# Optimization experiments

Measured on AMD Instinct MI355X. Metric: run time of the kernel, lower is better.

Reference implementation:

```python
import jax, jax.numpy as jnp
import numpy as np

N, E, IN, OUT = 50000, 1600000, 64, 64
DIM, K = 2, 5          # pseudo-coordinate dim, kernel size per dim
KP = K ** DIM          # 25 kernel weight matrices
S = 2 ** DIM           # 4 non-zero linear B-spline basis products per edge
# bit pattern per basis product: bits[s, d] in {0,1}
_BITS = np.array([[(s >> d) & 1 for d in range(DIM)] for s in range(S)], dtype=np.int32)
_OFFS = np.array([K ** (DIM - 1 - d) for d in range(DIM)], dtype=np.int32)  # row-major flatten


def setup_inputs() -> dict:
    key = jax.random.key(0)
    ks = jax.random.split(key, 6)
    x = jax.random.normal(ks[0], (N, IN), dtype=jnp.float32)
    edge_index = jax.random.randint(ks[1], (2, E), 0, N)
    pseudo = jax.random.uniform(ks[2], (E, DIM), dtype=jnp.float32)
    bnd = 1.0 / np.sqrt(KP * IN)  # matches uniform(size) init in reset_parameters
    weight = jax.random.uniform(ks[3], (KP, IN, OUT), dtype=jnp.float32, minval=-bnd, maxval=bnd)
    root_weight = jax.random.uniform(ks[4], (IN, OUT), dtype=jnp.float32, minval=-bnd, maxval=bnd)
    bias = jax.random.uniform(ks[5], (OUT,), dtype=jnp.float32, minval=-bnd, maxval=bnd)
    return {"x": x, "edge_index": edge_index, "pseudo": pseudo,
            "weight": weight, "root_weight": root_weight, "bias": bias}


def _basis_and_index(pseudo):
    # open B-spline, degree 1: scale by (K - 1)
    v = pseudo * jnp.asarray(K - 1, pseudo.dtype)          # [E, DIM]
    lo = jnp.floor(v)
    frac = v - lo                                          # [E, DIM]
    lo = lo.astype(jnp.int32)
    bits = jnp.asarray(_BITS)                              # [S, DIM]
    # basis[e, s] = prod_d (frac if bit else 1-frac)
    terms = jnp.where(bits[None].astype(bool), frac[:, None, :], 1.0 - frac[:, None, :])
    basis = jnp.prod(terms, axis=-1)                       # [E, S]
    idx_d = (lo[:, None, :] + bits[None]) % K              # [E, S, DIM]; wrap is harmless (basis=0 there)
    idx = jnp.sum(idx_d * jnp.asarray(_OFFS), axis=-1)     # [E, S] flat weight index in [0, KP)
    return basis, idx


def reference(x, edge_index, pseudo, weight, root_weight, bias):
    row, col = edge_index[0], edge_index[1]                # row = target, col = source
    basis, idx = _basis_and_index(pseudo)                  # [E,S], [E,S]
    x_src = x[col]                                         # [E, IN] gather
    # Accumulate basis-weighted source features per (target node, kernel index),
    # then apply the dense [KP, IN, OUT] weights once (same math, no [E,IN,OUT] blowup).
    acc = jnp.zeros((N * KP, IN), x.dtype)
    for s in range(S):  # S=4, fixed structural loop
        acc = acc + jax.ops.segment_sum(basis[:, s:s + 1] * x_src,
                                        row * KP + idx[:, s], num_segments=N * KP)
    out = jnp.einsum('nki,kio->no', acc.reshape(N, KP, IN), weight)  # [N, OUT]
    deg = jax.ops.segment_sum(jnp.ones((E,), x.dtype), row, num_segments=N)
    out = out / jnp.clip(deg, 1.0)[:, None]                # mean over neighbors (1/N(i))
    return out + x @ root_weight + bias
```

## Files before the change

### kernel.cpp

```cpp
#include <hip/hip_runtime.h>
#include <hip/hip_fp16.h>
#include <hip/hip_bf16.h>


#define NN    50000
#define EE    1600000
#define NPB   16
#define KD    1664
#define ASTB  1672
#define OFCAP 16384

#define NB    391
#define NSH   4
#define CCAP  1280
#define CSTR  16

#define REC_B 6250
#define XB_B  1563
#define WT_B  104

typedef unsigned short ushort_t;
typedef unsigned long long u64_t;
typedef __attribute__((ext_vector_type(8))) short short8;
typedef __attribute__((ext_vector_type(4))) float f32x4;

static __device__ __forceinline__ ushort_t f2bf(float f) {
  union { float f; unsigned u; } v; v.f = f;
  return (ushort_t)((v.u + 0x7fffu + ((v.u >> 16) & 1u)) >> 16);
}
static __device__ __forceinline__ unsigned pk2bf(float a, float b) {
  __hip_bfloat162 h = __float22bfloat162_rn(make_float2(a, b));
  union { __hip_bfloat162 h; unsigned u; } cv; cv.h = h; return cv.u;
}
union S8 { short8 s; unsigned u[4]; };

__global__ __launch_bounds__(256) void k_prep(
    const int* __restrict__ ei, const float* __restrict__ pseudo,
    int* __restrict__ ccur, uint2* __restrict__ coarse,
    const float* __restrict__ x, ushort_t* __restrict__ xb,
    const float* __restrict__ w, const float* __restrict__ root,
    ushort_t* __restrict__ wt, int useXB) {
  const int b = blockIdx.x;
  const int tid = threadIdx.x;
  if (b < REC_B) {
    int e = b * 256 + tid;
    int row = ei[e], col = ei[EE + e];
    float2 pv = ((const float2*)pseudo)[e];
    float v0 = pv.x * 4.0f, v1 = pv.y * 4.0f;
    unsigned h0 = __half_as_ushort(__float2half(v0));
    unsigned h1 = __half_as_ushort(__float2half(v1));
    int c4 = (row >> 7) * NSH + (tid & (NSH - 1));
    int slot = atomicAdd(&ccur[c4 * CSTR], 1);
    if (slot < CCAP)
      coarse[(size_t)c4 * CCAP + slot] =
          make_uint2((unsigned)col | ((unsigned)(row & 127) << 16), h0 | (h1 << 16));
  } else if (b < REC_B + XB_B) {
    if (!useXB) return;
    int t = (b - REC_B) * 256 + tid;
    if (t < NN * 8) {
      const float4* xp = (const float4*)x + (size_t)t * 2;
      float4 aa = xp[0], bb = xp[1];
      S8 o;
      o.u[0] = pk2bf(aa.x, aa.y); o.u[1] = pk2bf(aa.z, aa.w);
      o.u[2] = pk2bf(bb.x, bb.y); o.u[3] = pk2bf(bb.z, bb.w);
      ((short8*)xb)[t] = o.s;
    }
  } else {
    int t = (b - REC_B - XB_B) * 256 + tid;
    int idx = t * 4;
    if (idx < 64 * KD) {
      int o = idx / KD, k = idx - o * KD;
#pragma unroll
      for (int q = 0; q < 4; ++q) {
        int kk = k + q;
        int kp = kk >> 6, c = kk & 63;
        int fi = 4 * (c & 15) + (c >> 4);
        wt[idx + q] = (kp < 25) ? f2bf(w[(kp * 64 + fi) * 64 + o])
                                : f2bf(root[fi * 64 + o]);
      }
    }
  }
}

__global__ __launch_bounds__(256) void k_sort(
    const int* __restrict__ ccur, const uint2* __restrict__ coarse,
    uint2* __restrict__ recs2, int* __restrict__ degA,
    uint4* __restrict__ ofl, int* __restrict__ ofc) {
  __shared__ int cnt[128], lpos[128];
  const int c = blockIdx.x, tid = threadIdx.x;
  if (tid < 128) cnt[tid] = 0;
  __syncthreads();
  const int pc = c * NSH;
  for (int s = 0; s < NSH; ++s) {
    int n = min(ccur[(pc + s) * CSTR], CCAP);
    const uint2* seg = coarse + (size_t)(pc + s) * CCAP;
    for (int i = tid; i < n; i += 256) atomicAdd(&cnt[(seg[i].x >> 16) & 127], 1);
  }
  __syncthreads();
  if (tid < 128) {
    int row = c * 128 + tid;
    lpos[tid] = row * 64;
    if (row < NN) degA[row] = cnt[tid];
  }
  for (int i = tid; i < 128 * 64; i += 256) {
    int r7 = i >> 6, sl = i & 63;
    int row = c * 128 + r7;
    if (row < NN && sl >= cnt[r7])
      recs2[(size_t)row * 64 + sl] = make_uint2(0u, 0x7C007C00u);
  }
  __syncthreads();
  for (int s = 0; s < NSH; ++s) {
    int n = min(ccur[(pc + s) * CSTR], CCAP);
    const uint2* seg = coarse + (size_t)(pc + s) * CCAP;
    for (int i = tid; i < n; i += 256) {
      uint2 r = seg[i];
      int r7 = (r.x >> 16) & 127;
      int dst = atomicAdd(&lpos[r7], 1);
      int sl = dst - (c * 128 + r7) * 64;
      if (sl < 64) {
        recs2[dst] = make_uint2(r.x & 0xFFFFu, r.y);
      } else {
        int o = atomicAdd(ofc, 1);
        if (o < OFCAP) {
          float v0 = __half2float(__ushort_as_half((ushort_t)(r.y & 0xFFFFu)));
          float v1 = __half2float(__ushort_as_half((ushort_t)(r.y >> 16)));
          ofl[o] = make_uint4((unsigned)(c * 128 + r7), r.x & 0xFFFFu,
                              __float_as_uint(v0), __float_as_uint(v1));
        }
      }
    }
  }
}

static __device__ __forceinline__ void issue8(
    const ushort_t* __restrict__ xb, const unsigned (&vo)[8], u64_t (&g)[8]) {
  asm volatile(
      "global_load_dwordx2 %[o0], %[a0], %[sb]\n\t"
      "global_load_dwordx2 %[o1], %[a1], %[sb]\n\t"
      "global_load_dwordx2 %[o2], %[a2], %[sb]\n\t"
      "global_load_dwordx2 %[o3], %[a3], %[sb]\n\t"
      "global_load_dwordx2 %[o4], %[a4], %[sb]\n\t"
      "global_load_dwordx2 %[o5], %[a5], %[sb]\n\t"
      "global_load_dwordx2 %[o6], %[a6], %[sb]\n\t"
      "global_load_dwordx2 %[o7], %[a7], %[sb]\n\t"
      : [o0] "=&v"(g[0]), [o1] "=&v"(g[1]), [o2] "=&v"(g[2]), [o3] "=&v"(g[3]),
        [o4] "=&v"(g[4]), [o5] "=&v"(g[5]), [o6] "=&v"(g[6]), [o7] "=&v"(g[7])
      : [a0] "v"(vo[0]), [a1] "v"(vo[1]), [a2] "v"(vo[2]), [a3] "v"(vo[3]),
        [a4] "v"(vo[4]), [a5] "v"(vo[5]), [a6] "v"(vo[6]), [a7] "v"(vo[7]),
        [sb] "s"(xb));
}
static __device__ __forceinline__ void wait8(u64_t (&g)[8]) {
  asm volatile("s_waitcnt vmcnt(0)"
               : "+v"(g[0]), "+v"(g[1]), "+v"(g[2]), "+v"(g[3]),
                 "+v"(g[4]), "+v"(g[5]), "+v"(g[6]), "+v"(g[7]));
}

static __device__ __forceinline__ void vo8(
    unsigned wx, int base, int quad, int m15, unsigned (&vo)[8]) {
#pragma unroll
  for (int j = 0; j < 8; ++j) {
    unsigned c = (unsigned)__shfl((int)wx, base + quad * 8 + j);
    vo[j] = (c << 7) + (unsigned)(m15 << 3);
  }
}

static __device__ __forceinline__ void hats8(
    unsigned wy, int base, int quad, int m15,
    float r0f, float c0f, float r1f, float c1f, S8& aT0, S8& aT1) {
#pragma unroll
  for (int p = 0; p < 4; ++p) {
    float a0[2], a1[2];
#pragma unroll
    for (int q = 0; q < 2; ++q) {
      unsigned pv = (unsigned)__shfl((int)wy, base + quad * 8 + 2 * p + q);
      float v0 = __half2float(__ushort_as_half((ushort_t)(pv & 0xFFFFu)));
      float v1 = __half2float(__ushort_as_half((ushort_t)(pv >> 16)));
      a0[q] = fmaxf(0.f, 1.f - fabsf(v0 - r0f)) * fmaxf(0.f, 1.f - fabsf(v1 - c0f));
      a1[q] = fmaxf(0.f, 1.f - fabsf(v0 - r1f)) * fmaxf(0.f, 1.f - fabsf(v1 - c1f));
    }
    aT0.u[p] = pk2bf(a0[0], a0[1]);
    aT1.u[p] = pk2bf(a1[0], a1[1]);
  }
}

static __device__ __forceinline__ void packmfma(
    const u64_t (&g)[8], const S8& aT0, const S8& aT1, f32x4 (&acc)[2][4]) {
  S8 bT[4];
#pragma unroll
  for (int p = 0; p < 4; ++p) {
    unsigned lo0 = (unsigned)g[2 * p],     hi0 = (unsigned)(g[2 * p] >> 32);
    unsigned lo1 = (unsigned)g[2 * p + 1], hi1 = (unsigned)(g[2 * p + 1] >> 32);
    bT[0].u[p] = (lo0 & 0xFFFFu) | (lo1 << 16);
    bT[1].u[p] = (lo0 >> 16)     | (lo1 & 0xFFFF0000u);
    bT[2].u[p] = (hi0 & 0xFFFFu) | (hi1 << 16);
    bT[3].u[p] = (hi0 >> 16)     | (hi1 & 0xFFFF0000u);
  }
  __builtin_amdgcn_s_setprio(1);
#pragma unroll
  for (int t = 0; t < 4; ++t) {
    acc[0][t] = __builtin_amdgcn_mfma_f32_16x16x32_bf16(aT0.s, bT[t].s, acc[0][t], 0, 0, 0);
    acc[1][t] = __builtin_amdgcn_mfma_f32_16x16x32_bf16(aT1.s, bT[t].s, acc[1][t], 0, 0, 0);
  }
  __builtin_amdgcn_s_setprio(0);
}

static __device__ __forceinline__ void node_bf16(
    unsigned wx, unsigned wy, int m, int quad, int m15,
    float r0f, float c0f, float r1f, float c1f,
    const ushort_t* __restrict__ xb, f32x4 (&acc)[2][4]) {
  if (m > 32) {
    unsigned vo0[8], vo1[8];
    u64_t g0[8], g1[8];
    vo8(wx, 0, quad, m15, vo0);
    issue8(xb, vo0, g0);
    vo8(wx, 32, quad, m15, vo1);
    issue8(xb, vo1, g1);
    S8 aT0_0, aT1_0, aT0_1, aT1_1;
    hats8(wy, 0,  quad, m15, r0f, c0f, r1f, c1f, aT0_0, aT1_0);
    hats8(wy, 32, quad, m15, r0f, c0f, r1f, c1f, aT0_1, aT1_1);
    __builtin_amdgcn_sched_barrier(0);
    wait8(g0); wait8(g1);
    packmfma(g0, aT0_0, aT1_0, acc);
    packmfma(g1, aT0_1, aT1_1, acc);
  } else {
    unsigned vo0[8];
    u64_t g0[8];
    vo8(wx, 0, quad, m15, vo0);
    issue8(xb, vo0, g0);
    S8 aT0, aT1;
    hats8(wy, 0, quad, m15, r0f, c0f, r1f, c1f, aT0, aT1);
    __builtin_amdgcn_sched_barrier(0);
    wait8(g0);
    packmfma(g0, aT0, aT1, acc);
  }
}

static __device__ __forceinline__ void replay_ofl(
    const uint4* __restrict__ ofl, int ofcv, int node, int quad, int m15,
    float r0f, float c0f, float r1f, float c1f,
    const float* __restrict__ x, f32x4 (&acc)[2][4]) {
  for (int i = 0; i < ofcv; ++i) {
    uint4 r = ofl[i];
    if ((int)r.x != node) continue;
    float v0 = __uint_as_float(r.z), v1 = __uint_as_float(r.w);
    float h00 = fmaxf(0.f, 1.f - fabsf(v0 - r0f));
    float h01 = fmaxf(0.f, 1.f - fabsf(v1 - c0f));
    float h10 = fmaxf(0.f, 1.f - fabsf(v0 - r1f));
    float h11 = fmaxf(0.f, 1.f - fabsf(v1 - c1f));
    float mk = (quad == 0) ? 1.0f : 0.0f;
    S8 aT0, aT1, bT[4];
#pragma unroll
    for (int p = 0; p < 4; ++p) { aT0.u[p] = 0; aT1.u[p] = 0; }
    aT0.u[0] = pk2bf(h00 * h01 * mk, 0.0f);
    aT1.u[0] = pk2bf(h10 * h11 * mk, 0.0f);
    float4 xv = *(const float4*)(x + (size_t)r.y * 64 + (m15 << 2));
    float fv[4] = {xv.x, xv.y, xv.z, xv.w};
#pragma unroll
    for (int t = 0; t < 4; ++t)
#pragma unroll
      for (int p = 0; p < 4; ++p) bT[t].u[p] = pk2bf(fv[t], fv[t]);
#pragma unroll
    for (int t = 0; t < 4; ++t) {
      acc[0][t] = __builtin_amdgcn_mfma_f32_16x16x32_bf16(aT0.s, bT[t].s, acc[0][t], 0, 0, 0);
      acc[1][t] = __builtin_amdgcn_mfma_f32_16x16x32_bf16(aT1.s, bT[t].s, acc[1][t], 0, 0, 0);
    }
  }
}

static __device__ __forceinline__ void do_chunk_f32(
    const uint2 (&rq)[8], int kb, int m, int quad, int m15,
    float r0f, float c0f, float r1f, float c1f,
    const float* __restrict__ x, f32x4 (&acc)[2][4]) {
  unsigned cj[8], pj[8];
#pragma unroll
  for (int j = 0; j < 8; ++j) {
    cj[j] = min(rq[j].x, (unsigned)(NN - 1));
    pj[j] = rq[j].y;
  }
  float gf[4][8];
#pragma unroll
  for (int j = 0; j < 8; ++j) {
    float4 v = *(const float4*)(x + ((size_t)cj[j] << 6) + (m15 << 2));
    gf[0][j] = v.x; gf[1][j] = v.y; gf[2][j] = v.z; gf[3][j] = v.w;
  }
  S8 aT0, aT1, bT[4];
#pragma unroll
  for (int p = 0; p < 4; ++p) {
    float a0[2], a1[2];
#pragma unroll
    for (int q = 0; q < 2; ++q) {
      int j = 2 * p + q;
      unsigned pv = pj[j];
      float v0 = __half2float(__ushort_as_half((ushort_t)(pv & 0xFFFFu)));
      float v1 = __half2float(__ushort_as_half((ushort_t)(pv >> 16)));
      bool ok = (kb + quad * 8 + j) < m;
      float p0 = fmaxf(0.f, 1.f - fabsf(v0 - r0f)) * fmaxf(0.f, 1.f - fabsf(v1 - c0f));
      float p1 = fmaxf(0.f, 1.f - fabsf(v0 - r1f)) * fmaxf(0.f, 1.f - fabsf(v1 - c1f));
      a0[q] = ok ? p0 : 0.0f;
      a1[q] = ok ? p1 : 0.0f;
    }
    aT0.u[p] = pk2bf(a0[0], a0[1]);
    aT1.u[p] = pk2bf(a1[0], a1[1]);
  }
#pragma unroll
  for (int p = 0; p < 4; ++p)
#pragma unroll
    for (int t = 0; t < 4; ++t)
      bT[t].u[p] = pk2bf(gf[t][2 * p], gf[t][2 * p + 1]);
#pragma unroll
  for (int t = 0; t < 4; ++t) {
    acc[0][t] = __builtin_amdgcn_mfma_f32_16x16x32_bf16(aT0.s, bT[t].s, acc[0][t], 0, 0, 0);
    acc[1][t] = __builtin_amdgcn_mfma_f32_16x16x32_bf16(aT1.s, bT[t].s, acc[1][t], 0, 0, 0);
  }
}

static __device__ __forceinline__ void spill_acc(
    ushort_t* accS, int row, int quad, int m15, const f32x4 (&acc)[2][4]) {
#pragma unroll
  for (int mt = 0; mt < 2; ++mt)
#pragma unroll
    for (int r = 0; r < 4; ++r) {
      int kp = mt * 16 + quad * 4 + r;
      if (kp < 25) {
#pragma unroll
        for (int nt = 0; nt < 4; ++nt)
          accS[row * ASTB + kp * 64 + nt * 16 + m15] = f2bf(acc[mt][nt][r]);
      }
    }
}

template <bool XBF>
__global__ __launch_bounds__(512, 4) void k_main(
    const uint2* __restrict__ recs2, const int* __restrict__ degA,
    const uint4* __restrict__ ofl, const int* __restrict__ ofc,
    const float* __restrict__ x, const ushort_t* __restrict__ xb,
    const ushort_t* __restrict__ wt, const float* __restrict__ bias,
    float* __restrict__ out) {
  __shared__ ushort_t accS[NPB * ASTB];
  __shared__ float    outp[2 * NPB * 64];
  __shared__ float    sinv[NPB];
  const int tid = threadIdx.x;
  const int lane = tid & 63;
  const int w = tid >> 6;
  const int nb = blockIdx.x * NPB;

  const int m15 = lane & 15, quad = lane >> 4;
  const float r0f = (float)(m15 / 5),        c0f = (float)(m15 % 5);
  const float r1f = (float)((16 + m15) / 5), c1f = (float)((16 + m15) % 5);
  const int fl = 4 * m15 + quad;

  const int rowA = w << 1, rowB = rowA + 1;
  const int nodeA = nb + rowA, nodeB = nb + rowB;

  const int mA = degA[nodeA], mB = degA[nodeB];
  uint2 wA = recs2[(size_t)nodeA * 64 + lane];
  uint2 wB = recs2[(size_t)nodeB * 64 + lane];
  const float rxA = x[(size_t)nodeA * 64 + fl];
  const float rxB = x[(size_t)nodeB * 64 + fl];
  const int ofcv = min(ofc[0], OFCAP);

  const float dcfA = (float)max(mA, 1), dcfB = (float)max(mB, 1);
  if (lane == 0) { sinv[rowA] = 1.0f / dcfA; sinv[rowB] = 1.0f / dcfB; }
  accS[rowA * ASTB + 1600 + lane] = f2bf(rxA * dcfA);
  accS[rowB * ASTB + 1600 + lane] = f2bf(rxB * dcfB);

  f32x4 acc[2][4];
#pragma unroll
  for (int a = 0; a < 2; ++a)
#pragma unroll
    for (int b = 0; b < 4; ++b) acc[a][b] = (f32x4){0.f, 0.f, 0.f, 0.f};

  if (XBF) {
    node_bf16(wA.x, wA.y, mA, quad, m15, r0f, c0f, r1f, c1f, xb, acc);
    if (ofcv) replay_ofl(ofl, ofcv, nodeA, quad, m15, r0f, c0f, r1f, c1f, x, acc);
    spill_acc(accS, rowA, quad, m15, acc);
#pragma unroll
    for (int a = 0; a < 2; ++a)
#pragma unroll
      for (int b = 0; b < 4; ++b) acc[a][b] = (f32x4){0.f, 0.f, 0.f, 0.f};
    node_bf16(wB.x, wB.y, mB, quad, m15, r0f, c0f, r1f, c1f, xb, acc);
    if (ofcv) replay_ofl(ofl, ofcv, nodeB, quad, m15, r0f, c0f, r1f, c1f, x, acc);
    spill_acc(accS, rowB, quad, m15, acc);
  } else {
    for (int e0 = 0; e0 < min(mA, 64); e0 += 32) {
      uint2 rq[8];
#pragma unroll
      for (int j = 0; j < 8; ++j) rq[j] = recs2[(size_t)nodeA * 64 + e0 + quad * 8 + j];
      do_chunk_f32(rq, e0, mA, quad, m15, r0f, c0f, r1f, c1f, x, acc);
    }
    if (ofcv) replay_ofl(ofl, ofcv, nodeA, quad, m15, r0f, c0f, r1f, c1f, x, acc);
    spill_acc(accS, rowA, quad, m15, acc);
#pragma unroll
    for (int a = 0; a < 2; ++a)
#pragma unroll
      for (int b = 0; b < 4; ++b) acc[a][b] = (f32x4){0.f, 0.f, 0.f, 0.f};
    for (int e0 = 0; e0 < min(mB, 64); e0 += 32) {
      uint2 rq[8];
#pragma unroll
      for (int j = 0; j < 8; ++j) rq[j] = recs2[(size_t)nodeB * 64 + e0 + quad * 8 + j];
      do_chunk_f32(rq, e0, mB, quad, m15, r0f, c0f, r1f, c1f, x, acc);
    }
    if (ofcv) replay_ofl(ofl, ofcv, nodeB, quad, m15, r0f, c0f, r1f, c1f, x, acc);
    spill_acc(accS, rowB, quad, m15, acc);
  }
  __syncthreads();

  {
    const int ntile = w & 3, kh = w >> 2;
    const int m2 = lane & 15, quad2 = lane >> 4;
    const int nn2 = ntile * 16 + m2;
    f32x4 d = {0.0f, 0.0f, 0.0f, 0.0f};
    const ushort_t* ab = &accS[m2 * ASTB + kh * 832 + quad2 * 8];
    const ushort_t* wb = &wt[(size_t)nn2 * KD + kh * 832 + quad2 * 8];
    short8 bfs[6];
#pragma unroll
    for (int kk = 0; kk < 6; ++kk) bfs[kk] = *(const short8*)(wb + kk * 32);
#pragma unroll
    for (int kk = 0; kk < 26; ++kk) {
      short8 af = *(const short8*)(ab + kk * 32);
      d = __builtin_amdgcn_mfma_f32_16x16x32_bf16(af, bfs[kk % 6], d, 0, 0, 0);
      if (kk + 6 < 26) bfs[kk % 6] = *(const short8*)(wb + (kk + 6) * 32);
    }
#pragma unroll
    for (int r = 0; r < 4; ++r)
      outp[kh * (NPB * 64) + (quad2 * 4 + r) * 64 + ntile * 16 + m2] = d[r];
  }
  __syncthreads();

  {
#pragma unroll
    for (int h = 0; h < 2; ++h) {
      int i = h * 512 + tid;
      int nl = i >> 6, o = i & 63;
      float conv = outp[i] + outp[NPB * 64 + i];
      out[(size_t)(nb + nl) * 64 + o] = conv * sinv[nl] + bias[o];
    }
  }
}

__global__ void k_sentinel(float* __restrict__ out) {
  int i = blockIdx.x * 256 + threadIdx.x;
  if (i < NN * 64) out[i] = 1000.0f;
}

extern "C" void kernel_launch(void* const* d_in, const int* in_sizes, int n_in,
                              void* d_out, int out_size, void* d_ws, size_t ws_size,
                              hipStream_t stream) {
  const float* x      = (const float*)d_in[0];
  const int*   ei     = (const int*)d_in[1];
  const float* pseudo = (const float*)d_in[2];
  const float* w      = (const float*)d_in[3];
  const float* root   = (const float*)d_in[4];
  const float* bias   = (const float*)d_in[5];
  float* out = (float*)d_out;
  (void)in_sizes; (void)n_in; (void)out_size;

  char* ws = (char*)d_ws;
  size_t off = 0;
  auto alloc = [&](size_t bytes) { size_t r = off; off += (bytes + 511) & ~(size_t)511; return r; };
  ushort_t* wt     = (ushort_t*)(ws + alloc((size_t)64 * KD * 2));
  int*      ccur   = (int*)(ws + alloc((size_t)(NB * NSH * CSTR + 16) * 4));
  int*      ofcp   = ccur + NB * NSH * CSTR;
  int*      degA   = (int*)(ws + alloc((size_t)NN * 4));
  uint4*    ofl    = (uint4*)(ws + alloc((size_t)OFCAP * 16));
  uint2*    recs2  = (uint2*)(ws + alloc((size_t)NN * 64 * 8));
  uint2*    coarse = (uint2*)(ws + alloc((size_t)NB * NSH * CCAP * 8));
  size_t baseNeed  = off;
  ushort_t* xb     = (ushort_t*)(ws + alloc((size_t)NN * 64 * 2));
  size_t fullNeed  = off;

  if (ws_size < baseNeed) {
    k_sentinel<<<(NN * 64 + 255) / 256, 256, 0, stream>>>(out);
    return;
  }
  const int useXB = (ws_size >= fullNeed) ? 1 : 0;

  hipMemsetAsync(ccur, 0, (size_t)(NB * NSH * CSTR + 16) * 4, stream);
  k_prep<<<REC_B + XB_B + WT_B, 256, 0, stream>>>(ei, pseudo, ccur, coarse,
                                                  x, xb, w, root, wt, useXB);
  k_sort<<<NB, 256, 0, stream>>>(ccur, coarse, recs2, degA, ofl, ofcp);
  if (useXB)
    k_main<true><<<NN / NPB, 512, 0, stream>>>(recs2, degA, ofl, ofcp, x, xb, wt, bias, out);
  else
    k_main<false><<<NN / NPB, 512, 0, stream>>>(recs2, degA, ofl, ofcp, x, xb, wt, bias, out);
}
```

Measured before the change: 305.0 us.

## Software-pipeline bf16 gather loads across both nodes with partial vmcnt waits

Replaces the per-node gather routine with a flat, software-pipelined sequence. Node B's gathers are issued while node A's MFMAs run, and partial s_waitcnt vmcnt(8) lets each 8-load batch be consumed while the next stays in flight. It also drops the m>32 branch and always issues both 32-edge halves, adding loads for low-degree nodes. The out-of-line replay and spill for node A now run while B's loads are pending, which also hides that latency.

```diff
diff --git a/kernel.cpp b/kernel.cpp
--- a/kernel.cpp
+++ b/kernel.cpp
@@ -149,7 +149,12 @@
         [a4] "v"(vo[4]), [a5] "v"(vo[5]), [a6] "v"(vo[6]), [a7] "v"(vo[7]),
         [sb] "s"(xb));
 }
-static __device__ __forceinline__ void wait8(u64_t (&g)[8]) {
+static __device__ __forceinline__ void wait_vm8(u64_t (&g)[8]) {
+  asm volatile("s_waitcnt vmcnt(8)"
+               : "+v"(g[0]), "+v"(g[1]), "+v"(g[2]), "+v"(g[3]),
+                 "+v"(g[4]), "+v"(g[5]), "+v"(g[6]), "+v"(g[7]));
+}
+static __device__ __forceinline__ void wait_vm0(u64_t (&g)[8]) {
   asm volatile("s_waitcnt vmcnt(0)"
                : "+v"(g[0]), "+v"(g[1]), "+v"(g[2]), "+v"(g[3]),
                  "+v"(g[4]), "+v"(g[5]), "+v"(g[6]), "+v"(g[7]));
@@ -202,37 +207,6 @@
     acc[1][t] = __builtin_amdgcn_mfma_f32_16x16x32_bf16(aT1.s, bT[t].s, acc[1][t], 0, 0, 0);
   }
   __builtin_amdgcn_s_setprio(0);
-}
-
-static __device__ __forceinline__ void node_bf16(
-    unsigned wx, unsigned wy, int m, int quad, int m15,
-    float r0f, float c0f, float r1f, float c1f,
-    const ushort_t* __restrict__ xb, f32x4 (&acc)[2][4]) {
-  if (m > 32) {
-    unsigned vo0[8], vo1[8];
-    u64_t g0[8], g1[8];
-    vo8(wx, 0, quad, m15, vo0);
-    issue8(xb, vo0, g0);
-    vo8(wx, 32, quad, m15, vo1);
-    issue8(xb, vo1, g1);
-    S8 aT0_0, aT1_0, aT0_1, aT1_1;
-    hats8(wy, 0,  quad, m15, r0f, c0f, r1f, c1f, aT0_0, aT1_0);
-    hats8(wy, 32, quad, m15, r0f, c0f, r1f, c1f, aT0_1, aT1_1);
-    __builtin_amdgcn_sched_barrier(0);
-    wait8(g0); wait8(g1);
-    packmfma(g0, aT0_0, aT1_0, acc);
-    packmfma(g1, aT0_1, aT1_1, acc);
-  } else {
-    unsigned vo0[8];
-    u64_t g0[8];
-    vo8(wx, 0, quad, m15, vo0);
-    issue8(xb, vo0, g0);
-    S8 aT0, aT1;
-    hats8(wy, 0, quad, m15, r0f, c0f, r1f, c1f, aT0, aT1);
-    __builtin_amdgcn_sched_barrier(0);
-    wait8(g0);
-    packmfma(g0, aT0, aT1, acc);
-  }
 }
 
 static __device__ __forceinline__ void replay_ofl(
@@ -371,14 +345,38 @@
     for (int b = 0; b < 4; ++b) acc[a][b] = (f32x4){0.f, 0.f, 0.f, 0.f};
 
   if (XBF) {
-    node_bf16(wA.x, wA.y, mA, quad, m15, r0f, c0f, r1f, c1f, xb, acc);
+    asm volatile("" :: "v"(wA.x), "v"(wA.y), "v"(wB.x), "v"(wB.y));
+
+    u64_t g0[8], g1[8];
+    unsigned vo[8];
+    S8 aT0, aT1;
+
+    vo8(wA.x, 0, quad, m15, vo);  issue8(xb, vo, g0);
+    vo8(wA.x, 32, quad, m15, vo); issue8(xb, vo, g1);
+    hats8(wA.y, 0, quad, m15, r0f, c0f, r1f, c1f, aT0, aT1);
+    __builtin_amdgcn_sched_barrier(0);
+    wait_vm8(g0);
+    packmfma(g0, aT0, aT1, acc);
+    vo8(wB.x, 0, quad, m15, vo);  issue8(xb, vo, g0);
+    hats8(wA.y, 32, quad, m15, r0f, c0f, r1f, c1f, aT0, aT1);
+    __builtin_amdgcn_sched_barrier(0);
+    wait_vm8(g1);
+    packmfma(g1, aT0, aT1, acc);
+    vo8(wB.x, 32, quad, m15, vo); issue8(xb, vo, g1);
     if (ofcv) replay_ofl(ofl, ofcv, nodeA, quad, m15, r0f, c0f, r1f, c1f, x, acc);
     spill_acc(accS, rowA, quad, m15, acc);
 #pragma unroll
     for (int a = 0; a < 2; ++a)
 #pragma unroll
       for (int b = 0; b < 4; ++b) acc[a][b] = (f32x4){0.f, 0.f, 0.f, 0.f};
-    node_bf16(wB.x, wB.y, mB, quad, m15, r0f, c0f, r1f, c1f, xb, acc);
+    hats8(wB.y, 0, quad, m15, r0f, c0f, r1f, c1f, aT0, aT1);
+    __builtin_amdgcn_sched_barrier(0);
+    wait_vm8(g0);
+    packmfma(g0, aT0, aT1, acc);
+    hats8(wB.y, 32, quad, m15, r0f, c0f, r1f, c1f, aT0, aT1);
+    __builtin_amdgcn_sched_barrier(0);
+    wait_vm0(g1);
+    packmfma(g1, aT0, aT1, acc);
     if (ofcv) replay_ofl(ofl, ofcv, nodeB, quad, m15, r0f, c0f, r1f, c1f, x, acc);
     spill_acc(accS, rowB, quad, m15, acc);
   } else {
```

After: 307.6 us. About the same (+0.8%).
